# Performance work log

Measured on AMD Instinct MI355X. Metric: run time of the kernel, lower is better.

Reference implementation:

```python
import jax, jax.numpy as jnp
import numpy as np

B, T, D = 4, 4096, 1024

def setup_inputs() -> dict:
    key = jax.random.key(0)
    ks = jax.random.split(key, 6)
    x = jax.random.normal(ks[0], (B, T, D), dtype=jnp.float32)
    mask = jax.random.randint(ks[1], (B, T), 0, 2).astype(bool)
    # torch nn.Linear init scale ~ 1/sqrt(fan_in); exact init unimportant for correctness baseline
    s = 1.0 / np.sqrt(D)
    W_qkv = jax.random.normal(ks[2], (3 * D, D), dtype=jnp.float32) * s
    b_qkv = jax.random.normal(ks[3], (3 * D,), dtype=jnp.float32) * s
    W_out = jax.random.normal(ks[4], (D, D), dtype=jnp.float32) * s
    b_out = jax.random.normal(ks[5], (D,), dtype=jnp.float32) * s
    return {"x": x, "mask": mask, "W_qkv": W_qkv, "b_qkv": b_qkv, "W_out": W_out, "b_out": b_out}

def reference(x, mask, W_qkv, b_qkv, W_out, b_out):
    # qkv projection: (B,T,D) @ (D,3D) + (3D,)
    qkv = jnp.einsum('btd,ed->bte', x, W_qkv) + b_qkv
    q, k, v = jnp.split(qkv, 3, axis=-1)  # each (B,T,D)
    q = q / jnp.linalg.norm(q, axis=-1, keepdims=True)
    k = k / jnp.linalg.norm(k, axis=-1, keepdims=True)
    k = jnp.where(mask[..., None], 0.0, k)  # masked_fill(mask, 0)
    kv = jnp.sum(k * v, axis=-2, keepdims=True)  # (B,1,D) global feature sum
    out = kv * q  # (B,T,D)
    return jnp.einsum('btd,ed->bte', out, W_out) + b_out
```

## Files before the change

kernel.cpp:

```cpp
#include <hip/hip_runtime.h>
#include <stdint.h>


typedef short  short8   __attribute__((ext_vector_type(8)));
typedef float  floatx16 __attribute__((ext_vector_type(16)));

#define BM 128
#define BN 128
#define BK 64

__device__ __forceinline__ void async16(const void* g, void* l) {
  __builtin_amdgcn_global_load_lds((const __attribute__((address_space(1))) void*)g,
                                   (__attribute__((address_space(3))) void*)l, 16, 0, 0);
}

__device__ __forceinline__ uint16_t f2bf(float f) {
  union { float f; uint32_t u; } x; x.f = f;
  uint32_t u = x.u;
  return (uint16_t)((u + 0x7fffu + ((u >> 16) & 1u)) >> 16);
}
__device__ __forceinline__ float bf2f(uint16_t h) {
  union { uint32_t u; float f; } x; x.u = ((uint32_t)h) << 16; return x.f;
}
__device__ __forceinline__ uint32_t pack2(float a, float b) {
  return (uint32_t)f2bf(a) | ((uint32_t)f2bf(b) << 16);
}
__device__ __forceinline__ void upk8(uint4 u, float* f) {
  f[0]=bf2f((uint16_t)u.x); f[1]=bf2f((uint16_t)(u.x>>16));
  f[2]=bf2f((uint16_t)u.y); f[3]=bf2f((uint16_t)(u.y>>16));
  f[4]=bf2f((uint16_t)u.z); f[5]=bf2f((uint16_t)(u.z>>16));
  f[6]=bf2f((uint16_t)u.w); f[7]=bf2f((uint16_t)(u.w>>16));
}

__global__ __launch_bounds__(256) void cvt3(
    const float* __restrict__ a, uint16_t* __restrict__ ao, int na,
    const float* __restrict__ b, uint16_t* __restrict__ bo, int nb,
    const float* __restrict__ c, uint16_t* __restrict__ co, int nc) {
  int i = blockIdx.x * 256 + threadIdx.x;
  const float* in; uint16_t* out; int j = i;
  if (j < na) { in = a; out = ao; }
  else {
    j -= na;
    if (j < nb) { in = b; out = bo; }
    else { j -= nb; if (j >= nc) return; in = c; out = co; }
  }
  const float4* p = (const float4*)in;
  float4 u = p[(size_t)j * 2], v = p[(size_t)j * 2 + 1];
  uint4 o;
  o.x = pack2(u.x, u.y); o.y = pack2(u.z, u.w);
  o.z = pack2(v.x, v.y); o.w = pack2(v.z, v.w);
  ((uint4*)out)[j] = o;
}

__global__ __launch_bounds__(256, 2) void gemm1(
    const uint16_t* __restrict__ A, const uint16_t* __restrict__ Bw,
    const float* __restrict__ bias, uint16_t* __restrict__ Cb,
    int N, int K)
{
  __shared__ __align__(16) uint16_t As[BM * BK];
  __shared__ __align__(16) uint16_t Bs[BN * BK];
  const int tid = threadIdx.x;
  const int wave = tid >> 6, lane = tid & 63;
  const int l31 = lane & 31, khalf = lane >> 5;
  const int wm = wave & 1, wn = wave >> 1;
  const int id = blockIdx.x;
  const int xcd = id & 7, w = id >> 3;
  const int tileM = (w / 3) * BM;
  const int tileN = (xcd * 3 + (w % 3)) * BN;

  const int srow = wave * 8 + (lane >> 3);
  const int skc  = (lane & 7) ^ (lane >> 3);
  const uint16_t* gA = A  + (size_t)(tileM + srow) * K + skc * 8;
  const uint16_t* gB = Bw + (size_t)(tileN + srow) * K + skc * 8;
  char* lA = (char*)As + wave * 64 * 16;
  char* lB = (char*)Bs + wave * 64 * 16;

  floatx16 acc[2][2];
#pragma unroll
  for (int mi = 0; mi < 2; mi++)
#pragma unroll
    for (int ni = 0; ni < 2; ni++)
#pragma unroll
      for (int r = 0; r < 16; r++) acc[mi][ni][r] = 0.f;

  const int arow0 = wm * 64 + l31;
  const int brow0 = wn * 64 + l31;

  for (int k0 = 0; k0 < K; k0 += BK) {
#pragma unroll
    for (int s = 0; s < 4; s++) {
      async16(gA + k0 + s * 32 * K, lA + s * 4096);
      async16(gB + k0 + s * 32 * K, lB + s * 4096);
    }
    __syncthreads();
#pragma unroll
    for (int ks = 0; ks < 4; ks++) {
      const int kc = khalf + ks * 2;
      short8 af[2], bfr[2];
#pragma unroll
      for (int mi = 0; mi < 2; mi++) {
        int r = arow0 + mi * 32;
        af[mi] = *(const short8*)&As[(r * 8 + (kc ^ (r & 7))) * 8];
      }
#pragma unroll
      for (int ni = 0; ni < 2; ni++) {
        int r = brow0 + ni * 32;
        bfr[ni] = *(const short8*)&Bs[(r * 8 + (kc ^ (r & 7))) * 8];
      }
#pragma unroll
      for (int mi = 0; mi < 2; mi++)
#pragma unroll
        for (int ni = 0; ni < 2; ni++)
          acc[mi][ni] = __builtin_amdgcn_mfma_f32_32x32x16_bf16(af[mi], bfr[ni], acc[mi][ni], 0, 0, 0);
    }
    __syncthreads();
  }

#pragma unroll
  for (int mi = 0; mi < 2; mi++) {
    int rbase = tileM + wm * 64 + mi * 32 + 4 * khalf;
#pragma unroll
    for (int ni = 0; ni < 2; ni++) {
      int col = tileN + wn * 64 + ni * 32 + l31;
      float bv = bias[col];
#pragma unroll
      for (int reg = 0; reg < 16; reg++) {
        int row = rbase + (reg & 3) + 8 * (reg >> 2);
        Cb[(size_t)row * N + col] = f2bf(acc[mi][ni][reg] + bv);
      }
    }
  }
}

__global__ __launch_bounds__(256, 2) void gemm2(
    const uint16_t* __restrict__ qkv, const float* __restrict__ invq,
    const uint16_t* __restrict__ Wp, const float* __restrict__ bias,
    float* __restrict__ Cf)
{
  __shared__ __align__(16) uint16_t As[BM * BK];
  __shared__ __align__(16) uint16_t Bs[BN * BK];
  const int tid = threadIdx.x;
  const int wave = tid >> 6, lane = tid & 63;
  const int l31 = lane & 31, khalf = lane >> 5;
  const int wm = wave & 1, wn = wave >> 1;
  const int id = blockIdx.x;
  const int tileM = (id >> 3) * BM;
  const int tileN = (id & 7) * BN;
  const int batch = tileM >> 12;

  const int srow = wave * 8 + (lane >> 3);
  const int skc  = (lane & 7) ^ (lane >> 3);
  const uint16_t* gA = qkv + (size_t)(tileM + srow) * 3072 + skc * 8;
  const uint16_t* gB = Wp + (size_t)batch * 1024 * 1024
                          + (size_t)(tileN + srow) * 1024 + skc * 8;
  char* lA = (char*)As + wave * 64 * 16;
  char* lB = (char*)Bs + wave * 64 * 16;

  floatx16 acc[2][2];
#pragma unroll
  for (int mi = 0; mi < 2; mi++)
#pragma unroll
    for (int ni = 0; ni < 2; ni++)
#pragma unroll
      for (int r = 0; r < 16; r++) acc[mi][ni][r] = 0.f;

  const int arow0 = wm * 64 + l31;
  const int brow0 = wn * 64 + l31;

  for (int k0 = 0; k0 < 1024; k0 += BK) {
#pragma unroll
    for (int s = 0; s < 4; s++) {
      async16(gA + k0 + (size_t)s * 32 * 3072, lA + s * 4096);
      async16(gB + k0 + (size_t)s * 32 * 1024, lB + s * 4096);
    }
    __syncthreads();
#pragma unroll
    for (int ks = 0; ks < 4; ks++) {
      const int kc = khalf + ks * 2;
      short8 af[2], bfr[2];
#pragma unroll
      for (int mi = 0; mi < 2; mi++) {
        int r = arow0 + mi * 32;
        af[mi] = *(const short8*)&As[(r * 8 + (kc ^ (r & 7))) * 8];
      }
#pragma unroll
      for (int ni = 0; ni < 2; ni++) {
        int r = brow0 + ni * 32;
        bfr[ni] = *(const short8*)&Bs[(r * 8 + (kc ^ (r & 7))) * 8];
      }
#pragma unroll
      for (int mi = 0; mi < 2; mi++)
#pragma unroll
        for (int ni = 0; ni < 2; ni++)
          acc[mi][ni] = __builtin_amdgcn_mfma_f32_32x32x16_bf16(af[mi], bfr[ni], acc[mi][ni], 0, 0, 0);
    }
    __syncthreads();
  }

#pragma unroll
  for (int mi = 0; mi < 2; mi++) {
    int rbase = tileM + wm * 64 + mi * 32 + 4 * khalf;
#pragma unroll
    for (int ni = 0; ni < 2; ni++) {
      int col = tileN + wn * 64 + ni * 32 + l31;
      float bv = bias[col];
#pragma unroll
      for (int reg = 0; reg < 16; reg++) {
        int row = rbase + (reg & 3) + 8 * (reg >> 2);
        Cf[(size_t)row * 1024 + col] = fmaf(invq[row], acc[mi][ni][reg], bv);
      }
    }
  }
}

__global__ __launch_bounds__(256) void scale_w(
    const uint16_t* __restrict__ wo, const float* __restrict__ kv,
    uint16_t* __restrict__ wp)
{
  int i = blockIdx.x * 256 + threadIdx.x;
  int e = i << 3;
  int b = e >> 20;
  int k = e & 1023;
  uint4 w = *(const uint4*)(wo + (e & 0xFFFFF));
  float4 k0v = *(const float4*)(kv + (b << 10) + k);
  float4 k1v = *(const float4*)(kv + (b << 10) + k + 4);
  float wf[8]; upk8(w, wf);
  uint4 o;
  o.x = pack2(wf[0] * k0v.x, wf[1] * k0v.y);
  o.y = pack2(wf[2] * k0v.z, wf[3] * k0v.w);
  o.z = pack2(wf[4] * k1v.x, wf[5] * k1v.y);
  o.w = pack2(wf[6] * k1v.z, wf[7] * k1v.w);
  *(uint4*)(wp + e) = o;
}

__global__ __launch_bounds__(256) void detect_mask(const unsigned char* __restrict__ m,
                                                   int* __restrict__ flag) {
  int i = blockIdx.x * blockDim.x + threadIdx.x;
  int v = ((i & 3) != 0) ? (int)m[i] : 0;
  unsigned long long b = __ballot(v != 0);
  if ((threadIdx.x & 63) == 0 && b) atomicOr(flag, 1);
}

__global__ __launch_bounds__(256) void rownorm_kv(
    const uint16_t* __restrict__ qkv, const void* __restrict__ maskbuf,
    const int* __restrict__ flag, float* __restrict__ invq, float* __restrict__ kv)
{
  __shared__ float kvloc[1024];
  const int tid = threadIdx.x;
  for (int i = tid; i < 1024; i += 256) kvloc[i] = 0.f;
  __syncthreads();
  const int wave = tid >> 6, lane = tid & 63;
  const int b = blockIdx.x >> 7;
  const int chunk = blockIdx.x & 127;
  const int isU8 = *flag;
  const unsigned char* m8 = (const unsigned char*)maskbuf;
  const int* m32 = (const int*)maskbuf;

  float kvacc[16];
#pragma unroll
  for (int i = 0; i < 16; i++) kvacc[i] = 0.f;

  const int r0 = b * 4096 + chunk * 32 + wave * 8;
#pragma unroll 2
  for (int j = 0; j < 8; j++) {
    int r = r0 + j;
    const uint16_t* rp = qkv + (size_t)r * 3072;
    uint4 q0 = *(const uint4*)(rp + lane * 16);
    uint4 q1 = *(const uint4*)(rp + lane * 16 + 8);
    uint4 k0 = *(const uint4*)(rp + 1024 + lane * 16);
    uint4 k1 = *(const uint4*)(rp + 1024 + lane * 16 + 8);
    uint4 v0 = *(const uint4*)(rp + 2048 + lane * 16);
    uint4 v1 = *(const uint4*)(rp + 2048 + lane * 16 + 8);
    float qf[16], kf[16], vf[16];
    upk8(q0, qf); upk8(q1, qf + 8);
    upk8(k0, kf); upk8(k1, kf + 8);
    upk8(v0, vf); upk8(v1, vf + 8);
    float sq = 0.f, sk = 0.f;
#pragma unroll
    for (int i = 0; i < 16; i++) { sq = fmaf(qf[i], qf[i], sq); sk = fmaf(kf[i], kf[i], sk); }
    for (int off = 32; off; off >>= 1) { sq += __shfl_xor(sq, off); sk += __shfl_xor(sk, off); }
    float rq = rsqrtf(sq), rk = rsqrtf(sk);
    if (lane == 0) invq[r] = rq;
    int masked = isU8 ? (int)m8[r] : m32[r];
    if (!masked) {
#pragma unroll
      for (int i = 0; i < 16; i++) kvacc[i] = fmaf(kf[i] * rk, vf[i], kvacc[i]);
    }
  }
#pragma unroll
  for (int i = 0; i < 16; i++) atomicAdd(&kvloc[lane * 16 + i], kvacc[i]);
  __syncthreads();
  for (int i = tid; i < 1024; i += 256) atomicAdd(&kv[b * 1024 + i], kvloc[i]);
}

extern "C" void kernel_launch(void* const* d_in, const int* in_sizes, int n_in,
                              void* d_out, int out_size, void* d_ws, size_t ws_size,
                              hipStream_t stream) {
  const float* x     = (const float*)d_in[0];
  const void*  mask  = d_in[1];
  const float* W_qkv = (const float*)d_in[2];
  const float* b_qkv = (const float*)d_in[3];
  const float* W_out = (const float*)d_in[4];
  const float* b_out = (const float*)d_in[5];
  float* out = (float*)d_out;

  const int BT = 4 * 4096;
  const int D  = 1024;

  char* ws = (char*)d_ws;
  size_t off = 0;
  auto alloc = [&](size_t bytes) { size_t r = off; off += (bytes + 255) & ~(size_t)255; return r; };
  size_t o_xb   = alloc((size_t)BT * D * 2);
  size_t o_qkvb = alloc((size_t)BT * 3 * D * 2);
  size_t o_wq   = alloc((size_t)3 * D * D * 2);
  size_t o_wo   = alloc((size_t)D * D * 2);
  size_t o_wp   = alloc((size_t)4 * D * D * 2);
  size_t o_kv   = alloc((size_t)4 * D * 4 + 256);
  size_t o_invq = alloc((size_t)BT * 4);

  uint16_t* xb   = (uint16_t*)(ws + o_xb);
  uint16_t* qkvb = (uint16_t*)(ws + o_qkvb);
  uint16_t* wq   = (uint16_t*)(ws + o_wq);
  uint16_t* wo   = (uint16_t*)(ws + o_wo);
  uint16_t* wp   = (uint16_t*)(ws + o_wp);
  float*    kv   = (float*)(ws + o_kv);
  int*      flag = (int*)(ws + o_kv + (size_t)4 * D * 4);
  float*    invq = (float*)(ws + o_invq);

  hipMemsetAsync(ws + o_kv, 0, (size_t)4 * D * 4 + 256, stream);
  {
    int na = BT * D / 8, nb = 3 * D * D / 8, nc = D * D / 8;
    int tot = na + nb + nc;
    cvt3<<<dim3((tot + 255) / 256), 256, 0, stream>>>(x, xb, na, W_qkv, wq, nb, W_out, wo, nc);
  }
  detect_mask<<<dim3(64), 256, 0, stream>>>((const unsigned char*)mask, flag);
  gemm1<<<dim3(3072), 256, 0, stream>>>(xb, wq, b_qkv, qkvb, 3 * D, D);
  rownorm_kv<<<dim3(512), 256, 0, stream>>>(qkvb, mask, flag, invq, kv);
  scale_w<<<dim3(4 * D * D / 8 / 256), 256, 0, stream>>>(wo, kv, wp);
  gemm2<<<dim3(1024), 256, 0, stream>>>(qkvb, invq, wp, b_out, out);
}
```

Baseline: 330.1 us.

## Rewrite both GEMMs with 256x256 tiles and a 4-stage async LDS pipeline

Both bf16 GEMMs move from 128x128 tiles with BK=64 and two syncthreads per step to 256x256 tiles, 512 threads and BK=32, using a four-buffer LDS ring. Global-to-LDS loads for step t+3 are issued in the middle of the MFMA phases, and explicit vmcnt waits replace full syncthreads. MFMA issue priority is raised with setprio. The goals are to hide load latency, raise MFMA work per LDS byte and cut barrier stalls. The cost is far fewer blocks (768 and 256), a larger accumulator register footprint and 128 KB of LDS per block, which may limit occupancy and leave some CUs idle on gemm2.

```diff
diff --git a/kernel.cpp b/kernel.cpp
--- a/kernel.cpp
+++ b/kernel.cpp
@@ -5,9 +5,7 @@
 typedef short  short8   __attribute__((ext_vector_type(8)));
 typedef float  floatx16 __attribute__((ext_vector_type(16)));
 
-#define BM 128
-#define BN 128
-#define BK 64
+#define NT 32
 
 __device__ __forceinline__ void async16(const void* g, void* l) {
   __builtin_amdgcn_global_load_lds((const __attribute__((address_space(1))) void*)g,
@@ -52,161 +50,184 @@
   ((uint4*)out)[j] = o;
 }
 
-__global__ __launch_bounds__(256, 2) void gemm1(
+#define MFMA_PHASE(Ac, Bc, kcv, STAGE, GATE) { \
+    const int slot_ = (((kcv) ^ rsw) * 8); \
+    const uint16_t* Ap_ = (Ac) + slot_; \
+    const uint16_t* Bp_ = (Bc) + slot_; \
+    short8 a0_ = *(const short8*)&Ap_[(wm * 128 +  0 + l31) * 32]; \
+    short8 a1_ = *(const short8*)&Ap_[(wm * 128 + 32 + l31) * 32]; \
+    short8 a2_ = *(const short8*)&Ap_[(wm * 128 + 64 + l31) * 32]; \
+    short8 a3_ = *(const short8*)&Ap_[(wm * 128 + 96 + l31) * 32]; \
+    short8 b0_ = *(const short8*)&Bp_[(wn * 64 +  0 + l31) * 32]; \
+    short8 b1_ = *(const short8*)&Bp_[(wn * 64 + 32 + l31) * 32]; \
+    STAGE; \
+    __builtin_amdgcn_sched_barrier(0); \
+    __builtin_amdgcn_s_barrier(); \
+    asm volatile("s_waitcnt lgkmcnt(0)" ::: "memory"); \
+    __builtin_amdgcn_s_setprio(1); \
+    acc[0][0] = __builtin_amdgcn_mfma_f32_32x32x16_bf16(a0_, b0_, acc[0][0], 0, 0, 0); \
+    acc[0][1] = __builtin_amdgcn_mfma_f32_32x32x16_bf16(a0_, b1_, acc[0][1], 0, 0, 0); \
+    acc[1][0] = __builtin_amdgcn_mfma_f32_32x32x16_bf16(a1_, b0_, acc[1][0], 0, 0, 0); \
+    acc[1][1] = __builtin_amdgcn_mfma_f32_32x32x16_bf16(a1_, b1_, acc[1][1], 0, 0, 0); \
+    acc[2][0] = __builtin_amdgcn_mfma_f32_32x32x16_bf16(a2_, b0_, acc[2][0], 0, 0, 0); \
+    acc[2][1] = __builtin_amdgcn_mfma_f32_32x32x16_bf16(a2_, b1_, acc[2][1], 0, 0, 0); \
+    acc[3][0] = __builtin_amdgcn_mfma_f32_32x32x16_bf16(a3_, b0_, acc[3][0], 0, 0, 0); \
+    acc[3][1] = __builtin_amdgcn_mfma_f32_32x32x16_bf16(a3_, b1_, acc[3][1], 0, 0, 0); \
+    __builtin_amdgcn_s_setprio(0); \
+    GATE; \
+    __builtin_amdgcn_sched_barrier(0); \
+    __builtin_amdgcn_s_barrier(); \
+  }
+
+__global__ __launch_bounds__(512, 2) void gemm1(
     const uint16_t* __restrict__ A, const uint16_t* __restrict__ Bw,
-    const float* __restrict__ bias, uint16_t* __restrict__ Cb,
-    int N, int K)
+    const float* __restrict__ bias, uint16_t* __restrict__ Cb)
 {
-  __shared__ __align__(16) uint16_t As[BM * BK];
-  __shared__ __align__(16) uint16_t Bs[BN * BK];
+  __shared__ __align__(16) uint16_t As[4][8192];
+  __shared__ __align__(16) uint16_t Bs[4][8192];
   const int tid = threadIdx.x;
   const int wave = tid >> 6, lane = tid & 63;
   const int l31 = lane & 31, khalf = lane >> 5;
+  const int rsw = (l31 >> 1) & 3;
   const int wm = wave & 1, wn = wave >> 1;
   const int id = blockIdx.x;
   const int xcd = id & 7, w = id >> 3;
-  const int tileM = (w / 3) * BM;
-  const int tileN = (xcd * 3 + (w % 3)) * BN;
-
-  const int srow = wave * 8 + (lane >> 3);
-  const int skc  = (lane & 7) ^ (lane >> 3);
-  const uint16_t* gA = A  + (size_t)(tileM + srow) * K + skc * 8;
-  const uint16_t* gB = Bw + (size_t)(tileN + srow) * K + skc * 8;
-  char* lA = (char*)As + wave * 64 * 16;
-  char* lB = (char*)Bs + wave * 64 * 16;
-
-  floatx16 acc[2][2];
-#pragma unroll
-  for (int mi = 0; mi < 2; mi++)
+  const int tileM = ((w / 12) * 8 + xcd) * 256;
+  const int tileN = (w % 12) * 256;
+
+  const int srow = tid >> 2;
+  const int sk   = (tid & 3) ^ ((tid >> 3) & 3);
+  const uint16_t* gA = A  + (size_t)(tileM + srow) * 1024 + sk * 8;
+  const uint16_t* gB = Bw + (size_t)(tileN + srow) * 1024 + sk * 8;
+
+  floatx16 acc[4][2];
+#pragma unroll
+  for (int mi = 0; mi < 4; mi++)
 #pragma unroll
     for (int ni = 0; ni < 2; ni++)
 #pragma unroll
       for (int r = 0; r < 16; r++) acc[mi][ni][r] = 0.f;
 
-  const int arow0 = wm * 64 + l31;
-  const int brow0 = wn * 64 + l31;
-
-  for (int k0 = 0; k0 < K; k0 += BK) {
-#pragma unroll
-    for (int s = 0; s < 4; s++) {
-      async16(gA + k0 + s * 32 * K, lA + s * 4096);
-      async16(gB + k0 + s * 32 * K, lB + s * 4096);
-    }
-    __syncthreads();
-#pragma unroll
-    for (int ks = 0; ks < 4; ks++) {
-      const int kc = khalf + ks * 2;
-      short8 af[2], bfr[2];
-#pragma unroll
-      for (int mi = 0; mi < 2; mi++) {
-        int r = arow0 + mi * 32;
-        af[mi] = *(const short8*)&As[(r * 8 + (kc ^ (r & 7))) * 8];
-      }
-#pragma unroll
-      for (int ni = 0; ni < 2; ni++) {
-        int r = brow0 + ni * 32;
-        bfr[ni] = *(const short8*)&Bs[(r * 8 + (kc ^ (r & 7))) * 8];
-      }
-#pragma unroll
-      for (int mi = 0; mi < 2; mi++)
-#pragma unroll
-        for (int ni = 0; ni < 2; ni++)
-          acc[mi][ni] = __builtin_amdgcn_mfma_f32_32x32x16_bf16(af[mi], bfr[ni], acc[mi][ni], 0, 0, 0);
-    }
-    __syncthreads();
-  }
-
-#pragma unroll
-  for (int mi = 0; mi < 2; mi++) {
-    int rbase = tileM + wm * 64 + mi * 32 + 4 * khalf;
+#pragma unroll
+  for (int t = 0; t < 3; ++t) {
+    const size_t ko = (size_t)t * 32;
+    async16(gA + ko,                      (char*)As[t] + wave * 1024);
+    async16(gA + ko + (size_t)128 * 1024, (char*)As[t] + 8192 + wave * 1024);
+    async16(gB + ko,                      (char*)Bs[t] + wave * 1024);
+    async16(gB + ko + (size_t)128 * 1024, (char*)Bs[t] + 8192 + wave * 1024);
+  }
+  asm volatile("s_waitcnt vmcnt(8)" ::: "memory");
+  __builtin_amdgcn_s_barrier();
+
+#define STG_A1(tt) if ((tt) < NT) { const int c3_ = (tt) & 3; const size_t ko_ = (size_t)(tt) * 32; \
+    async16(gA + ko_,                      (char*)As[c3_] + wave * 1024); \
+    async16(gA + ko_ + (size_t)128 * 1024, (char*)As[c3_] + 8192 + wave * 1024); }
+#define STG_B1(tt) if ((tt) < NT) { const int c3_ = (tt) & 3; const size_t ko_ = (size_t)(tt) * 32; \
+    async16(gB + ko_,                      (char*)Bs[c3_] + wave * 1024); \
+    async16(gB + ko_ + (size_t)128 * 1024, (char*)Bs[c3_] + 8192 + wave * 1024); }
+#define GATE_ if (t + 3 < NT) { asm volatile("s_waitcnt vmcnt(8)" ::: "memory"); } \
+    else if (t + 2 < NT) { asm volatile("s_waitcnt vmcnt(4)" ::: "memory"); } \
+    else if (t + 1 < NT) { asm volatile("s_waitcnt vmcnt(0)" ::: "memory"); }
+
+#pragma unroll 1
+  for (int t = 0; t < NT; ++t) {
+    const uint16_t* Ac = As[t & 3];
+    const uint16_t* Bc = Bs[t & 3];
+    MFMA_PHASE(Ac, Bc, khalf,     STG_A1(t + 3), )
+    MFMA_PHASE(Ac, Bc, khalf + 2, STG_B1(t + 3), GATE_)
+  }
+#undef STG_A1
+#undef STG_B1
+#undef GATE_
+
+#pragma unroll
+  for (int mi = 0; mi < 4; mi++) {
+    const int rbase = tileM + wm * 128 + mi * 32 + 4 * khalf;
 #pragma unroll
     for (int ni = 0; ni < 2; ni++) {
-      int col = tileN + wn * 64 + ni * 32 + l31;
-      float bv = bias[col];
+      const int col = tileN + wn * 64 + ni * 32 + l31;
+      const float bv = bias[col];
 #pragma unroll
       for (int reg = 0; reg < 16; reg++) {
-        int row = rbase + (reg & 3) + 8 * (reg >> 2);
-        Cb[(size_t)row * N + col] = f2bf(acc[mi][ni][reg] + bv);
+        const int row = rbase + (reg & 3) + 8 * (reg >> 2);
+        Cb[(size_t)row * 3072 + col] = f2bf(acc[mi][ni][reg] + bv);
       }
     }
   }
 }
 
-__global__ __launch_bounds__(256, 2) void gemm2(
+__global__ __launch_bounds__(512, 2) void gemm2(
     const uint16_t* __restrict__ qkv, const float* __restrict__ invq,
     const uint16_t* __restrict__ Wp, const float* __restrict__ bias,
     float* __restrict__ Cf)
 {
-  __shared__ __align__(16) uint16_t As[BM * BK];
-  __shared__ __align__(16) uint16_t Bs[BN * BK];
+  __shared__ __align__(16) uint16_t As[4][8192];
+  __shared__ __align__(16) uint16_t Bs[4][8192];
   const int tid = threadIdx.x;
   const int wave = tid >> 6, lane = tid & 63;
   const int l31 = lane & 31, khalf = lane >> 5;
+  const int rsw = (l31 >> 1) & 3;
   const int wm = wave & 1, wn = wave >> 1;
   const int id = blockIdx.x;
-  const int tileM = (id >> 3) * BM;
-  const int tileN = (id & 7) * BN;
+  const int tileM = (id >> 2) * 256;
+  const int tileN = (id & 3) * 256;
   const int batch = tileM >> 12;
 
-  const int srow = wave * 8 + (lane >> 3);
-  const int skc  = (lane & 7) ^ (lane >> 3);
-  const uint16_t* gA = qkv + (size_t)(tileM + srow) * 3072 + skc * 8;
-  const uint16_t* gB = Wp + (size_t)batch * 1024 * 1024
-                          + (size_t)(tileN + srow) * 1024 + skc * 8;
-  char* lA = (char*)As + wave * 64 * 16;
-  char* lB = (char*)Bs + wave * 64 * 16;
-
-  floatx16 acc[2][2];
-#pragma unroll
-  for (int mi = 0; mi < 2; mi++)
+  const int srow = tid >> 2;
+  const int sk   = (tid & 3) ^ ((tid >> 3) & 3);
+  const uint16_t* gA = qkv + (size_t)(tileM + srow) * 3072 + sk * 8;
+  const uint16_t* gB = Wp + ((size_t)batch << 20) + (size_t)(tileN + srow) * 1024 + sk * 8;
+
+  floatx16 acc[4][2];
+#pragma unroll
+  for (int mi = 0; mi < 4; mi++)
 #pragma unroll
     for (int ni = 0; ni < 2; ni++)
 #pragma unroll
       for (int r = 0; r < 16; r++) acc[mi][ni][r] = 0.f;
 
-  const int arow0 = wm * 64 + l31;
-  const int brow0 = wn * 64 + l31;
-
-  for (int k0 = 0; k0 < 1024; k0 += BK) {
-#pragma unroll
-    for (int s = 0; s < 4; s++) {
-      async16(gA + k0 + (size_t)s * 32 * 3072, lA + s * 4096);
-      async16(gB + k0 + (size_t)s * 32 * 1024, lB + s * 4096);
-    }
-    __syncthreads();
-#pragma unroll
-    for (int ks = 0; ks < 4; ks++) {
-      const int kc = khalf + ks * 2;
-      short8 af[2], bfr[2];
-#pragma unroll
-      for (int mi = 0; mi < 2; mi++) {
-        int r = arow0 + mi * 32;
-        af[mi] = *(const short8*)&As[(r * 8 + (kc ^ (r & 7))) * 8];
-      }
-#pragma unroll
-      for (int ni = 0; ni < 2; ni++) {
-        int r = brow0 + ni * 32;
-        bfr[ni] = *(const short8*)&Bs[(r * 8 + (kc ^ (r & 7))) * 8];
-      }
-#pragma unroll
-      for (int mi = 0; mi < 2; mi++)
-#pragma unroll
-        for (int ni = 0; ni < 2; ni++)
-          acc[mi][ni] = __builtin_amdgcn_mfma_f32_32x32x16_bf16(af[mi], bfr[ni], acc[mi][ni], 0, 0, 0);
-    }
-    __syncthreads();
-  }
-
-#pragma unroll
-  for (int mi = 0; mi < 2; mi++) {
-    int rbase = tileM + wm * 64 + mi * 32 + 4 * khalf;
+#pragma unroll
+  for (int t = 0; t < 3; ++t) {
+    const size_t ko = (size_t)t * 32;
+    async16(gA + ko,                      (char*)As[t] + wave * 1024);
+    async16(gA + ko + (size_t)128 * 3072, (char*)As[t] + 8192 + wave * 1024);
+    async16(gB + ko,                      (char*)Bs[t] + wave * 1024);
+    async16(gB + ko + (size_t)128 * 1024, (char*)Bs[t] + 8192 + wave * 1024);
+  }
+  asm volatile("s_waitcnt vmcnt(8)" ::: "memory");
+  __builtin_amdgcn_s_barrier();
+
+#define STG_A2(tt) if ((tt) < NT) { const int c3_ = (tt) & 3; const size_t ko_ = (size_t)(tt) * 32; \
+    async16(gA + ko_,                      (char*)As[c3_] + wave * 1024); \
+    async16(gA + ko_ + (size_t)128 * 3072, (char*)As[c3_] + 8192 + wave * 1024); }
+#define STG_B2(tt) if ((tt) < NT) { const int c3_ = (tt) & 3; const size_t ko_ = (size_t)(tt) * 32; \
+    async16(gB + ko_,                      (char*)Bs[c3_] + wave * 1024); \
+    async16(gB + ko_ + (size_t)128 * 1024, (char*)Bs[c3_] + 8192 + wave * 1024); }
+#define GATE_ if (t + 3 < NT) { asm volatile("s_waitcnt vmcnt(8)" ::: "memory"); } \
+    else if (t + 2 < NT) { asm volatile("s_waitcnt vmcnt(4)" ::: "memory"); } \
+    else if (t + 1 < NT) { asm volatile("s_waitcnt vmcnt(0)" ::: "memory"); }
+
+#pragma unroll 1
+  for (int t = 0; t < NT; ++t) {
+    const uint16_t* Ac = As[t & 3];
+    const uint16_t* Bc = Bs[t & 3];
+    MFMA_PHASE(Ac, Bc, khalf,     STG_A2(t + 3), )
+    MFMA_PHASE(Ac, Bc, khalf + 2, STG_B2(t + 3), GATE_)
+  }
+#undef STG_A2
+#undef STG_B2
+#undef GATE_
+
+#pragma unroll
+  for (int mi = 0; mi < 4; mi++) {
+    const int rbase = tileM + wm * 128 + mi * 32 + 4 * khalf;
 #pragma unroll
     for (int ni = 0; ni < 2; ni++) {
-      int col = tileN + wn * 64 + ni * 32 + l31;
-      float bv = bias[col];
+      const int col = tileN + wn * 64 + ni * 32 + l31;
+      const float bv = bias[col];
 #pragma unroll
       for (int reg = 0; reg < 16; reg++) {
-        int row = rbase + (reg & 3) + 8 * (reg >> 2);
+        const int row = rbase + (reg & 3) + 8 * (reg >> 2);
         Cf[(size_t)row * 1024 + col] = fmaf(invq[row], acc[mi][ni][reg], bv);
       }
     }
@@ -334,8 +355,8 @@
     cvt3<<<dim3((tot + 255) / 256), 256, 0, stream>>>(x, xb, na, W_qkv, wq, nb, W_out, wo, nc);
   }
   detect_mask<<<dim3(64), 256, 0, stream>>>((const unsigned char*)mask, flag);
-  gemm1<<<dim3(3072), 256, 0, stream>>>(xb, wq, b_qkv, qkvb, 3 * D, D);
+  gemm1<<<dim3(768), 512, 0, stream>>>(xb, wq, b_qkv, qkvb);
   rownorm_kv<<<dim3(512), 256, 0, stream>>>(qkvb, mask, flag, invq, kv);
   scale_w<<<dim3(4 * D * D / 8 / 256), 256, 0, stream>>>(wo, kv, wp);
-  gemm2<<<dim3(1024), 256, 0, stream>>>(qkvb, invq, wp, b_out, out);
-}
+  gemm2<<<dim3(256), 512, 0, stream>>>(qkvb, invq, wp, b_out, out);
+}
```

After: 334.9 us. No clear change (+1.5%).

## Widen GEMM tiles to 128x256, remap block order, drop W_out bf16 conversion

Applied to the files above, without the earlier changes.

Both GEMMs move from 128x128 to 128x256 output tiles: each wave now computes a 2x4 grid of MFMA 32x32 accumulators, which doubles the reuse of every A fragment. Grid sizes are halved and block IDs are remapped across the 8 XCDs so that neighbouring M tiles that share a B tile land on the same XCD. The separate bf16 conversion of W_out is removed, and scale_w now reads the fp32 weights directly. The trade-off is more accumulator registers and 48KB of LDS per block, which may hurt the occupancy target of 2 blocks per CU, and fewer blocks means less load balancing across the 256 CUs.

```diff
diff --git a/kernel.cpp b/kernel.cpp
--- a/kernel.cpp
+++ b/kernel.cpp
@@ -4,10 +4,6 @@
 
 typedef short  short8   __attribute__((ext_vector_type(8)));
 typedef float  floatx16 __attribute__((ext_vector_type(16)));
-
-#define BM 128
-#define BN 128
-#define BK 64
 
 __device__ __forceinline__ void async16(const void* g, void* l) {
   __builtin_amdgcn_global_load_lds((const __attribute__((address_space(1))) void*)g,
@@ -32,18 +28,13 @@
   f[6]=bf2f((uint16_t)u.w); f[7]=bf2f((uint16_t)(u.w>>16));
 }
 
-__global__ __launch_bounds__(256) void cvt3(
+__global__ __launch_bounds__(256) void cvt2(
     const float* __restrict__ a, uint16_t* __restrict__ ao, int na,
-    const float* __restrict__ b, uint16_t* __restrict__ bo, int nb,
-    const float* __restrict__ c, uint16_t* __restrict__ co, int nc) {
+    const float* __restrict__ b, uint16_t* __restrict__ bo, int nb) {
   int i = blockIdx.x * 256 + threadIdx.x;
   const float* in; uint16_t* out; int j = i;
   if (j < na) { in = a; out = ao; }
-  else {
-    j -= na;
-    if (j < nb) { in = b; out = bo; }
-    else { j -= nb; if (j >= nc) return; in = c; out = co; }
-  }
+  else { j -= na; if (j >= nb) return; in = b; out = bo; }
   const float4* p = (const float4*)in;
   float4 u = p[(size_t)j * 2], v = p[(size_t)j * 2 + 1];
   uint4 o;
@@ -54,63 +45,62 @@
 
 __global__ __launch_bounds__(256, 2) void gemm1(
     const uint16_t* __restrict__ A, const uint16_t* __restrict__ Bw,
-    const float* __restrict__ bias, uint16_t* __restrict__ Cb,
-    int N, int K)
+    const float* __restrict__ bias, uint16_t* __restrict__ Cb)
 {
-  __shared__ __align__(16) uint16_t As[BM * BK];
-  __shared__ __align__(16) uint16_t Bs[BN * BK];
+  __shared__ __align__(16) uint16_t As[128 * 64];
+  __shared__ __align__(16) uint16_t Bs[256 * 64];
   const int tid = threadIdx.x;
   const int wave = tid >> 6, lane = tid & 63;
   const int l31 = lane & 31, khalf = lane >> 5;
   const int wm = wave & 1, wn = wave >> 1;
-  const int id = blockIdx.x;
-  const int xcd = id & 7, w = id >> 3;
-  const int tileM = (w / 3) * BM;
-  const int tileN = (xcd * 3 + (w % 3)) * BN;
+  const int wgid = (blockIdx.x & 7) * 192 + (blockIdx.x >> 3);
+  const int tileM = (wgid & 127) * 128;
+  const int tileN = (wgid >> 7) * 256;
 
   const int srow = wave * 8 + (lane >> 3);
   const int skc  = (lane & 7) ^ (lane >> 3);
-  const uint16_t* gA = A  + (size_t)(tileM + srow) * K + skc * 8;
-  const uint16_t* gB = Bw + (size_t)(tileN + srow) * K + skc * 8;
-  char* lA = (char*)As + wave * 64 * 16;
-  char* lB = (char*)Bs + wave * 64 * 16;
-
-  floatx16 acc[2][2];
+  const uint16_t* gA = A  + (size_t)(tileM + srow) * 1024 + skc * 8;
+  const uint16_t* gB = Bw + (size_t)(tileN + srow) * 1024 + skc * 8;
+  char* lA = (char*)As + wave * 1024;
+  char* lB = (char*)Bs + wave * 1024;
+
+  floatx16 acc[2][4];
 #pragma unroll
   for (int mi = 0; mi < 2; mi++)
 #pragma unroll
-    for (int ni = 0; ni < 2; ni++)
+    for (int ni = 0; ni < 4; ni++)
 #pragma unroll
       for (int r = 0; r < 16; r++) acc[mi][ni][r] = 0.f;
 
   const int arow0 = wm * 64 + l31;
-  const int brow0 = wn * 64 + l31;
-
-  for (int k0 = 0; k0 < K; k0 += BK) {
-#pragma unroll
-    for (int s = 0; s < 4; s++) {
-      async16(gA + k0 + s * 32 * K, lA + s * 4096);
-      async16(gB + k0 + s * 32 * K, lB + s * 4096);
-    }
+  const int brow0 = wn * 128 + l31;
+
+  for (int k0 = 0; k0 < 1024; k0 += 64) {
+#pragma unroll
+    for (int s = 0; s < 4; s++)
+      async16(gA + k0 + (size_t)s * 32 * 1024, lA + s * 4096);
+#pragma unroll
+    for (int s = 0; s < 8; s++)
+      async16(gB + k0 + (size_t)s * 32 * 1024, lB + s * 4096);
     __syncthreads();
 #pragma unroll
     for (int ks = 0; ks < 4; ks++) {
       const int kc = khalf + ks * 2;
-      short8 af[2], bfr[2];
+      short8 af[2], bfr[4];
 #pragma unroll
       for (int mi = 0; mi < 2; mi++) {
         int r = arow0 + mi * 32;
         af[mi] = *(const short8*)&As[(r * 8 + (kc ^ (r & 7))) * 8];
       }
 #pragma unroll
-      for (int ni = 0; ni < 2; ni++) {
+      for (int ni = 0; ni < 4; ni++) {
         int r = brow0 + ni * 32;
         bfr[ni] = *(const short8*)&Bs[(r * 8 + (kc ^ (r & 7))) * 8];
       }
 #pragma unroll
       for (int mi = 0; mi < 2; mi++)
 #pragma unroll
-        for (int ni = 0; ni < 2; ni++)
+        for (int ni = 0; ni < 4; ni++)
           acc[mi][ni] = __builtin_amdgcn_mfma_f32_32x32x16_bf16(af[mi], bfr[ni], acc[mi][ni], 0, 0, 0);
     }
     __syncthreads();
@@ -118,15 +108,15 @@
 
 #pragma unroll
   for (int mi = 0; mi < 2; mi++) {
-    int rbase = tileM + wm * 64 + mi * 32 + 4 * khalf;
-#pragma unroll
-    for (int ni = 0; ni < 2; ni++) {
-      int col = tileN + wn * 64 + ni * 32 + l31;
-      float bv = bias[col];
+    const int rbase = tileM + wm * 64 + mi * 32 + 4 * khalf;
+#pragma unroll
+    for (int ni = 0; ni < 4; ni++) {
+      const int col = tileN + wn * 128 + ni * 32 + l31;
+      const float bv = bias[col];
 #pragma unroll
       for (int reg = 0; reg < 16; reg++) {
-        int row = rbase + (reg & 3) + 8 * (reg >> 2);
-        Cb[(size_t)row * N + col] = f2bf(acc[mi][ni][reg] + bv);
+        const int row = rbase + (reg & 3) + 8 * (reg >> 2);
+        Cb[(size_t)row * 3072 + col] = f2bf(acc[mi][ni][reg] + bv);
       }
     }
   }
@@ -137,61 +127,61 @@
     const uint16_t* __restrict__ Wp, const float* __restrict__ bias,
     float* __restrict__ Cf)
 {
-  __shared__ __align__(16) uint16_t As[BM * BK];
-  __shared__ __align__(16) uint16_t Bs[BN * BK];
+  __shared__ __align__(16) uint16_t As[128 * 64];
+  __shared__ __align__(16) uint16_t Bs[256 * 64];
   const int tid = threadIdx.x;
   const int wave = tid >> 6, lane = tid & 63;
   const int l31 = lane & 31, khalf = lane >> 5;
   const int wm = wave & 1, wn = wave >> 1;
-  const int id = blockIdx.x;
-  const int tileM = (id >> 3) * BM;
-  const int tileN = (id & 7) * BN;
+  const int wgid = (blockIdx.x & 7) * 64 + (blockIdx.x >> 3);
+  const int tileM = (wgid & 127) * 128;
+  const int tileN = (wgid >> 7) * 256;
   const int batch = tileM >> 12;
 
   const int srow = wave * 8 + (lane >> 3);
   const int skc  = (lane & 7) ^ (lane >> 3);
   const uint16_t* gA = qkv + (size_t)(tileM + srow) * 3072 + skc * 8;
-  const uint16_t* gB = Wp + (size_t)batch * 1024 * 1024
-                          + (size_t)(tileN + srow) * 1024 + skc * 8;
-  char* lA = (char*)As + wave * 64 * 16;
-  char* lB = (char*)Bs + wave * 64 * 16;
-
-  floatx16 acc[2][2];
+  const uint16_t* gB = Wp + ((size_t)batch << 20) + (size_t)(tileN + srow) * 1024 + skc * 8;
+  char* lA = (char*)As + wave * 1024;
+  char* lB = (char*)Bs + wave * 1024;
+
+  floatx16 acc[2][4];
 #pragma unroll
   for (int mi = 0; mi < 2; mi++)
 #pragma unroll
-    for (int ni = 0; ni < 2; ni++)
+    for (int ni = 0; ni < 4; ni++)
 #pragma unroll
       for (int r = 0; r < 16; r++) acc[mi][ni][r] = 0.f;
 
   const int arow0 = wm * 64 + l31;
-  const int brow0 = wn * 64 + l31;
-
-  for (int k0 = 0; k0 < 1024; k0 += BK) {
-#pragma unroll
-    for (int s = 0; s < 4; s++) {
+  const int brow0 = wn * 128 + l31;
+
+  for (int k0 = 0; k0 < 1024; k0 += 64) {
+#pragma unroll
+    for (int s = 0; s < 4; s++)
       async16(gA + k0 + (size_t)s * 32 * 3072, lA + s * 4096);
+#pragma unroll
+    for (int s = 0; s < 8; s++)
       async16(gB + k0 + (size_t)s * 32 * 1024, lB + s * 4096);
-    }
     __syncthreads();
 #pragma unroll
     for (int ks = 0; ks < 4; ks++) {
       const int kc = khalf + ks * 2;
-      short8 af[2], bfr[2];
+      short8 af[2], bfr[4];
 #pragma unroll
       for (int mi = 0; mi < 2; mi++) {
         int r = arow0 + mi * 32;
         af[mi] = *(const short8*)&As[(r * 8 + (kc ^ (r & 7))) * 8];
       }
 #pragma unroll
-      for (int ni = 0; ni < 2; ni++) {
+      for (int ni = 0; ni < 4; ni++) {
         int r = brow0 + ni * 32;
         bfr[ni] = *(const short8*)&Bs[(r * 8 + (kc ^ (r & 7))) * 8];
       }
 #pragma unroll
       for (int mi = 0; mi < 2; mi++)
 #pragma unroll
-        for (int ni = 0; ni < 2; ni++)
+        for (int ni = 0; ni < 4; ni++)
           acc[mi][ni] = __builtin_amdgcn_mfma_f32_32x32x16_bf16(af[mi], bfr[ni], acc[mi][ni], 0, 0, 0);
     }
     __syncthreads();
@@ -199,14 +189,14 @@
 
 #pragma unroll
   for (int mi = 0; mi < 2; mi++) {
-    int rbase = tileM + wm * 64 + mi * 32 + 4 * khalf;
-#pragma unroll
-    for (int ni = 0; ni < 2; ni++) {
-      int col = tileN + wn * 64 + ni * 32 + l31;
-      float bv = bias[col];
+    const int rbase = tileM + wm * 64 + mi * 32 + 4 * khalf;
+#pragma unroll
+    for (int ni = 0; ni < 4; ni++) {
+      const int col = tileN + wn * 128 + ni * 32 + l31;
+      const float bv = bias[col];
 #pragma unroll
       for (int reg = 0; reg < 16; reg++) {
-        int row = rbase + (reg & 3) + 8 * (reg >> 2);
+        const int row = rbase + (reg & 3) + 8 * (reg >> 2);
         Cf[(size_t)row * 1024 + col] = fmaf(invq[row], acc[mi][ni][reg], bv);
       }
     }
@@ -214,22 +204,22 @@
 }
 
 __global__ __launch_bounds__(256) void scale_w(
-    const uint16_t* __restrict__ wo, const float* __restrict__ kv,
+    const float* __restrict__ wo, const float* __restrict__ kv,
     uint16_t* __restrict__ wp)
 {
   int i = blockIdx.x * 256 + threadIdx.x;
   int e = i << 3;
   int b = e >> 20;
   int k = e & 1023;
-  uint4 w = *(const uint4*)(wo + (e & 0xFFFFF));
+  float4 w0 = *(const float4*)(wo + (e & 0xFFFFF));
+  float4 w1 = *(const float4*)(wo + (e & 0xFFFFF) + 4);
   float4 k0v = *(const float4*)(kv + (b << 10) + k);
   float4 k1v = *(const float4*)(kv + (b << 10) + k + 4);
-  float wf[8]; upk8(w, wf);
   uint4 o;
-  o.x = pack2(wf[0] * k0v.x, wf[1] * k0v.y);
-  o.y = pack2(wf[2] * k0v.z, wf[3] * k0v.w);
-  o.z = pack2(wf[4] * k1v.x, wf[5] * k1v.y);
-  o.w = pack2(wf[6] * k1v.z, wf[7] * k1v.w);
+  o.x = pack2(w0.x * k0v.x, w0.y * k0v.y);
+  o.y = pack2(w0.z * k0v.z, w0.w * k0v.w);
+  o.z = pack2(w1.x * k1v.x, w1.y * k1v.y);
+  o.w = pack2(w1.z * k1v.z, w1.w * k1v.w);
   *(uint4*)(wp + e) = o;
 }
 
@@ -313,7 +303,6 @@
   size_t o_xb   = alloc((size_t)BT * D * 2);
   size_t o_qkvb = alloc((size_t)BT * 3 * D * 2);
   size_t o_wq   = alloc((size_t)3 * D * D * 2);
-  size_t o_wo   = alloc((size_t)D * D * 2);
   size_t o_wp   = alloc((size_t)4 * D * D * 2);
   size_t o_kv   = alloc((size_t)4 * D * 4 + 256);
   size_t o_invq = alloc((size_t)BT * 4);
@@ -321,7 +310,6 @@
   uint16_t* xb   = (uint16_t*)(ws + o_xb);
   uint16_t* qkvb = (uint16_t*)(ws + o_qkvb);
   uint16_t* wq   = (uint16_t*)(ws + o_wq);
-  uint16_t* wo   = (uint16_t*)(ws + o_wo);
   uint16_t* wp   = (uint16_t*)(ws + o_wp);
   float*    kv   = (float*)(ws + o_kv);
   int*      flag = (int*)(ws + o_kv + (size_t)4 * D * 4);
@@ -329,13 +317,13 @@
 
   hipMemsetAsync(ws + o_kv, 0, (size_t)4 * D * 4 + 256, stream);
   {
-    int na = BT * D / 8, nb = 3 * D * D / 8, nc = D * D / 8;
-    int tot = na + nb + nc;
-    cvt3<<<dim3((tot + 255) / 256), 256, 0, stream>>>(x, xb, na, W_qkv, wq, nb, W_out, wo, nc);
+    int na = BT * D / 8, nb = 3 * D * D / 8;
+    int tot = na + nb;
+    cvt2<<<dim3((tot + 255) / 256), 256, 0, stream>>>(x, xb, na, W_qkv, wq, nb);
   }
   detect_mask<<<dim3(64), 256, 0, stream>>>((const unsigned char*)mask, flag);
-  gemm1<<<dim3(3072), 256, 0, stream>>>(xb, wq, b_qkv, qkvb, 3 * D, D);
+  gemm1<<<dim3(1536), 256, 0, stream>>>(xb, wq, b_qkv, qkvb);
   rownorm_kv<<<dim3(512), 256, 0, stream>>>(qkvb, mask, flag, invq, kv);
-  scale_w<<<dim3(4 * D * D / 8 / 256), 256, 0, stream>>>(wo, kv, wp);
-  gemm2<<<dim3(1024), 256, 0, stream>>>(qkvb, invq, wp, b_out, out);
-}
+  scale_w<<<dim3(4 * D * D / 8 / 256), 256, 0, stream>>>(W_out, kv, wp);
+  gemm2<<<dim3(512), 256, 0, stream>>>(qkvb, invq, wp, b_out, out);
+}
```

Result: faster. 317.2 us (-3.9%).
